# Kernel optimization log

Measured on AMD Instinct MI355X. Metric: run time of the kernel, lower is better.

## Reference

```python
import jax, jax.numpy as jnp
import numpy as np

COMMITMENT_COST = 0.25
NUM_EMBEDDINGS = 1024
EMBEDDING_DIM = 256


def setup_inputs() -> dict:
    key = jax.random.key(0)
    k1, k2 = jax.random.split(key)
    inputs = jax.random.normal(k1, (16, 4096, EMBEDDING_DIM), dtype=jnp.float32)
    embedding = jax.random.normal(k2, (NUM_EMBEDDINGS, EMBEDDING_DIM), dtype=jnp.float32)
    return {"inputs": inputs, "embedding": embedding}


def reference(inputs, embedding):
    input_shape = inputs.shape  # [B, T, D]
    D = embedding.shape[1]
    K = embedding.shape[0]
    flat = inputs.reshape(-1, D)  # [N, D]

    distances = (
        jnp.sum(flat * flat, axis=1, keepdims=True)
        + jnp.sum(embedding * embedding, axis=1)
        - 2.0 * jnp.matmul(flat, embedding.T)
    )

    encoding_indices = jnp.argmin(distances, axis=1)  # [N]
    encodings = jax.nn.one_hot(encoding_indices, K, dtype=jnp.float32)  # [N, K]

    # quantized = encodings @ embedding (a gather, expressed as in the original)
    quantized = embedding[encoding_indices].reshape(input_shape)

    # Commitment loss (quantized detached); EMA / codebook loss handled via EMA updates in training.
    e_latent_loss = jnp.mean((jax.lax.stop_gradient(quantized) - inputs) ** 2)
    vq_loss = COMMITMENT_COST * e_latent_loss

    # Straight-through estimator
    quantized_st = inputs + jax.lax.stop_gradient(quantized - inputs)

    avg_probs = jnp.mean(encodings, axis=0)  # [K]
    perplexity = jnp.exp(-jnp.sum(avg_probs * jnp.log(avg_probs + 1e-10)))

    return (vq_loss, quantized_st, perplexity, encodings, distances,
            encoding_indices[:, None])
```

## Files before the change

kernel.cpp:

```cpp
#include <hip/hip_runtime.h>
#include <hip/hip_fp16.h>
#include <stdint.h>

#define D 256
#define BM 128
#define BN 128
#define EPS 68

#define GLOBAL_AS __attribute__((address_space(1)))
#define LDS_AS    __attribute__((address_space(3)))

typedef _Float16 f16x8 __attribute__((ext_vector_type(8)));
typedef float f32x4 __attribute__((ext_vector_type(4)));

__device__ __forceinline__ void gload16(const unsigned short* g, unsigned short* l) {
    __builtin_amdgcn_global_load_lds((const GLOBAL_AS void*)g, (LDS_AS void*)l, 16, 0, 0);
}

__global__ void prep_kernel(const float* __restrict__ X, const float* __restrict__ E,
                            double* __restrict__ xn, double* __restrict__ en,
                            unsigned short* __restrict__ Xh, unsigned short* __restrict__ Xl,
                            unsigned short* __restrict__ Eh, unsigned short* __restrict__ El,
                            unsigned long long* __restrict__ keys,
                            unsigned int* __restrict__ hist, int N, int K)
{
    int gid  = blockIdx.x * blockDim.x + threadIdx.x;
    int wid  = gid >> 6;
    int lane = threadIdx.x & 63;
    if (wid < N + K) {
        bool isX = wid < N;
        int r = isX ? wid : wid - N;
        const float* src = isX ? (X + (size_t)r * D) : (E + (size_t)r * D);
        float4 v = *(const float4*)(src + lane * 4);
        double s = (double)v.x*v.x + (double)v.y*v.y + (double)v.z*v.z + (double)v.w*v.w;
        #pragma unroll
        for (int o = 32; o >= 1; o >>= 1) s += __shfl_xor(s, o, 64);

        ushort4 h4, l4;
        {
            __half h;
            h = __float2half_rn(v.x); h4.x = __half_as_ushort(h);
            l4.x = __half_as_ushort(__float2half_rn((v.x - __half2float(h)) * 4096.0f));
            h = __float2half_rn(v.y); h4.y = __half_as_ushort(h);
            l4.y = __half_as_ushort(__float2half_rn((v.y - __half2float(h)) * 4096.0f));
            h = __float2half_rn(v.z); h4.z = __half_as_ushort(h);
            l4.z = __half_as_ushort(__float2half_rn((v.z - __half2float(h)) * 4096.0f));
            h = __float2half_rn(v.w); h4.w = __half_as_ushort(h);
            l4.w = __half_as_ushort(__float2half_rn((v.w - __half2float(h)) * 4096.0f));
        }
        int p = r >> 7, ri = r & 127;
        int c = lane >> 3, g = lane & 7;
        int slot = g >> 1, hf = g & 1;
        int slot_r = (slot + (ri >> 1)) & 3;
        size_t off = ((size_t)(p * 8 + c) * 128 + ri) * 32 + slot_r * 8 + hf * 4;
        if (isX) {
            *(ushort4*)(Xh + off) = h4; *(ushort4*)(Xl + off) = l4;
            if (lane == 0) xn[r] = s;
        } else {
            *(ushort4*)(Eh + off) = h4; *(ushort4*)(El + off) = l4;
            if (lane == 0) en[r] = s;
        }
    }
    int stride = gridDim.x * blockDim.x;
    for (int i = gid; i < N; i += stride) keys[i] = 0xFFFFFFFFFFFFFFFFull;
    for (int i = gid; i < K; i += stride) hist[i] = 0u;
}

__global__ __launch_bounds__(256, 2) void dist_mfma(
    const unsigned short* __restrict__ Xh, const unsigned short* __restrict__ Xl,
    const unsigned short* __restrict__ Eh, const unsigned short* __restrict__ El,
    const double* __restrict__ xn, const double* __restrict__ en,
    float* __restrict__ dist, unsigned long long* __restrict__ keys,
    int N, int K)
{
    __shared__ alignas(16) unsigned short smem[2 * 4 * 4096];

    const int tid  = threadIdx.x;
    const int lane = tid & 63;
    const int wv   = tid >> 6;
    const int wrow = (wv & 1) * 64;
    const int wcol = (wv >> 1) * 64;

    const int flat = blockIdx.y * gridDim.x + blockIdx.x;
    const int nf   = (flat & 7) * ((int)(gridDim.x * gridDim.y) >> 3) + (flat >> 3);
    const int bx   = nf & 7;
    const int by   = nf >> 3;
    const int row0 = by * BM;
    const int col0 = bx * BN;

    const unsigned short* gA_h = Xh + (size_t)by * 32768;
    const unsigned short* gA_l = Xl + (size_t)by * 32768;
    const unsigned short* gB_h = Eh + (size_t)bx * 32768;
    const unsigned short* gB_l = El + (size_t)bx * 32768;

    f32x4 acc[4][4];
    f32x4 acr[4][4];
    #pragma unroll
    for (int i = 0; i < 4; ++i)
        #pragma unroll
        for (int j = 0; j < 4; ++j) { acc[i][j] = {0.f,0.f,0.f,0.f}; acr[i][j] = {0.f,0.f,0.f,0.f}; }

    const int toff = tid * 8;

    #define STAGE(c_, b_)                                                           \
    {                                                                               \
        const int co = (c_) * 4096;                                                 \
        unsigned short* lb = smem + (b_) * 16384;                                   \
        _Pragma("unroll")                                                           \
        for (int t = 0; t < 2; ++t) {                                               \
            gload16(gA_h + co + t*2048 + toff, lb +         t*2048 + toff);         \
            gload16(gA_l + co + t*2048 + toff, lb +  4096 + t*2048 + toff);         \
            gload16(gB_h + co + t*2048 + toff, lb +  8192 + t*2048 + toff);         \
            gload16(gB_l + co + t*2048 + toff, lb + 12288 + t*2048 + toff);         \
        }                                                                           \
    }

    const int fr = lane & 15;
    const int kq = lane >> 4;
    const int q  = kq;

    int offA[4], offB[4];
    #pragma unroll
    for (int i = 0; i < 4; ++i) {
        int rowA = wrow + i*16 + fr;
        offA[i] = rowA * 32 + ((kq + (rowA >> 1)) & 3) * 8;
        int rowB = wcol + i*16 + fr;
        offB[i] = rowB * 32 + ((kq + (rowB >> 1)) & 3) * 8;
    }

    STAGE(0, 0);
    asm volatile("s_waitcnt vmcnt(0)" ::: "memory");
    __builtin_amdgcn_s_barrier();
    __builtin_amdgcn_sched_barrier(0);

    for (int c = 0; c < 8; ++c) {
        const int b = c & 1;
        if (c < 7) {
            STAGE(c + 1, b ^ 1);
            asm volatile("s_waitcnt vmcnt(8)" ::: "memory");
        } else {
            asm volatile("s_waitcnt vmcnt(0)" ::: "memory");
        }
        __builtin_amdgcn_s_barrier();
        __builtin_amdgcn_sched_barrier(0);

        const unsigned short* buf = smem + b * 16384;
        f16x8 ah[4], bh[4], al[4], bl[4];
        #pragma unroll
        for (int i = 0; i < 4; ++i)
            ah[i] = *(const f16x8*)&buf[offA[i]];
        #pragma unroll
        for (int j = 0; j < 4; ++j)
            bh[j] = *(const f16x8*)&buf[8192 + offB[j]];
        #pragma unroll
        for (int i = 0; i < 4; ++i)
            #pragma unroll
            for (int j = 0; j < 4; ++j)
                acc[i][j] = __builtin_amdgcn_mfma_f32_16x16x32_f16(ah[i], bh[j], acc[i][j], 0, 0, 0);
        #pragma unroll
        for (int j = 0; j < 4; ++j)
            bl[j] = *(const f16x8*)&buf[12288 + offB[j]];
        #pragma unroll
        for (int i = 0; i < 4; ++i)
            #pragma unroll
            for (int j = 0; j < 4; ++j)
                acr[i][j] = __builtin_amdgcn_mfma_f32_16x16x32_f16(ah[i], bl[j], acr[i][j], 0, 0, 0);
        #pragma unroll
        for (int i = 0; i < 4; ++i)
            al[i] = *(const f16x8*)&buf[4096 + offA[i]];
        #pragma unroll
        for (int i = 0; i < 4; ++i)
            #pragma unroll
            for (int j = 0; j < 4; ++j)
                acr[i][j] = __builtin_amdgcn_mfma_f32_16x16x32_f16(al[i], bh[j], acr[i][j], 0, 0, 0);

        asm volatile("s_waitcnt lgkmcnt(0)" ::: "memory");
        __builtin_amdgcn_s_barrier();
        __builtin_amdgcn_sched_barrier(0);
    }

    float ecv[4];
    #pragma unroll
    for (int j = 0; j < 4; ++j) ecv[j] = (float)en[col0 + wcol + j*16 + fr];

    char* arena = (char*)smem + wv * 16384;

    {
        unsigned long long* kbuf = (unsigned long long*)arena;
        #pragma unroll
        for (int i = 0; i < 4; ++i) {
            #pragma unroll
            for (int r = 0; r < 4; ++r) {
                const int lr = i*16 + q*4 + r;
                unsigned long long bk = 0xFFFFFFFFFFFFFFFFull;
                #pragma unroll
                for (int j = 0; j < 4; ++j) {
                    float dotf = fmaf(acr[i][j][r], 0.000244140625f, acc[i][j][r]);
                    float m    = fmaf(-2.0f, dotf, ecv[j]);
                    uint32_t u = __float_as_uint(m);
                    u ^= ((uint32_t)((int32_t)u >> 31)) | 0x80000000u;
                    unsigned long long kk = ((unsigned long long)u << 32)
                                          | (unsigned)(col0 + wcol + j*16 + fr);
                    if (kk < bk) bk = kk;
                }
                kbuf[lr * 17 + fr] = bk;
            }
        }
        asm volatile("s_waitcnt lgkmcnt(0)" ::: "memory");
        unsigned long long best = 0xFFFFFFFFFFFFFFFFull;
        #pragma unroll
        for (int s = 0; s < 16; ++s) {
            unsigned long long v = kbuf[lane * 17 + s];
            if (v < best) best = v;
        }
        atomicMin(&keys[row0 + wrow + lane], best);
        asm volatile("s_waitcnt lgkmcnt(0)" ::: "memory");
    }

    {
        float xr32[4][4];
        #pragma unroll
        for (int i = 0; i < 4; ++i)
            #pragma unroll
            for (int r = 0; r < 4; ++r)
                xr32[i][r] = (float)xn[row0 + wrow + i*16 + q*4 + r];

        float* ebuf = (float*)arena;
        #pragma unroll
        for (int h = 0; h < 2; ++h) {
            #pragma unroll
            for (int i2 = 0; i2 < 2; ++i2) {
                const int i = h * 2 + i2;
                #pragma unroll
                for (int r = 0; r < 4; ++r) {
                    #pragma unroll
                    for (int j = 0; j < 4; ++j) {
                        float dotf = fmaf(acr[i][j][r], 0.000244140625f, acc[i][j][r]);
                        float dv   = fmaf(-2.0f, dotf, xr32[i][r] + ecv[j]);
                        ebuf[(i2*16 + q*4 + r) * EPS + j*16 + fr] = dv;
                    }
                }
            }
            asm volatile("s_waitcnt lgkmcnt(0)" ::: "memory");
            #pragma unroll
            for (int s = 0; s < 8; ++s) {
                const int rl = s*4 + q;
                float4 v = *(const float4*)&ebuf[rl * EPS + fr * 4];
                const int grow = row0 + wrow + h*32 + rl;
                *(float4*)&dist[(size_t)grow * K + col0 + wcol + fr*4] = v;
            }
            asm volatile("s_waitcnt lgkmcnt(0)" ::: "memory");
        }
    }
    #undef STAGE
}

__global__ void row_out(const float* __restrict__ X, const float* __restrict__ E,
                        const unsigned long long* __restrict__ keys,
                        float* __restrict__ quant, float* __restrict__ enc,
                        float* __restrict__ idxf, unsigned int* __restrict__ hist,
                        float* __restrict__ partials, int N, int K)
{
    int wid  = (blockIdx.x * blockDim.x + threadIdx.x) >> 6;
    int lane = threadIdx.x & 63;
    if (wid >= N) return;
    int idx = (int)(unsigned)(keys[wid] & 0xFFFFFFFFull);

    float4 x4 = *(const float4*)(X + (size_t)wid * D + lane*4);
    float4 q4 = *(const float4*)(E + (size_t)idx * D + lane*4);
    *(float4*)(quant + (size_t)wid * D + lane*4) = q4;
    float dx = q4.x-x4.x, dy = q4.y-x4.y, dz = q4.z-x4.z, dw = q4.w-x4.w;
    float s = dx*dx + dy*dy + dz*dz + dw*dw;
    #pragma unroll
    for (int o = 32; o >= 1; o >>= 1) s += __shfl_xor(s, o, 64);

    #pragma unroll
    for (int c = 0; c < 4; ++c) {
        int col = c * 256 + lane * 4;
        float4 v;
        v.x = (col + 0 == idx) ? 1.0f : 0.0f;
        v.y = (col + 1 == idx) ? 1.0f : 0.0f;
        v.z = (col + 2 == idx) ? 1.0f : 0.0f;
        v.w = (col + 3 == idx) ? 1.0f : 0.0f;
        *(float4*)(enc + (size_t)wid * K + col) = v;
    }
    if (lane == 0) {
        partials[wid] = s;
        idxf[wid] = (float)idx;
        atomicAdd(&hist[idx], 1u);
    }
}

__global__ void finalize_kernel(const float* __restrict__ partials,
                                const unsigned int* __restrict__ hist,
                                float* __restrict__ out_loss,
                                float* __restrict__ out_perp,
                                int N, int K)
{
    int tid = threadIdx.x;
    float ls = 0.0f;
    for (int i = tid; i < N; i += 1024) ls += partials[i];
    float ent = 0.0f;
    if (tid < K) {
        float p = (float)hist[tid] / (float)N;
        ent = p * logf(p + 1e-10f);
    }
    #pragma unroll
    for (int o = 32; o >= 1; o >>= 1) {
        ls  += __shfl_xor(ls,  o, 64);
        ent += __shfl_xor(ent, o, 64);
    }
    __shared__ float sl[16], se[16];
    int w = tid >> 6, lane = tid & 63;
    if (lane == 0) { sl[w] = ls; se[w] = ent; }
    __syncthreads();
    if (tid == 0) {
        float L = 0.0f, En = 0.0f;
        for (int i = 0; i < 16; ++i) { L += sl[i]; En += se[i]; }
        *out_loss = 0.25f * L / ((float)N * (float)D);
        *out_perp = expf(-En);
    }
}

extern "C" void kernel_launch(void* const* d_in, const int* in_sizes, int n_in,
                              void* d_out, int out_size, void* d_ws, size_t ws_size,
                              hipStream_t stream)
{
    const float* X = (const float*)d_in[0];
    const float* E = (const float*)d_in[1];
    const int N = in_sizes[0] / D;
    const int K = in_sizes[1] / D;
    float* out = (float*)d_out;

    const size_t O1 = 1;
    const size_t O2 = O1 + (size_t)N * D;
    const size_t O3 = O2 + 1;
    const size_t O4 = O3 + (size_t)N * K;
    const size_t O5 = O4 + (size_t)N * K;

    char* ws = (char*)d_ws;
    size_t off = 0;
    auto alloc = [&](size_t bytes) -> void* {
        void* p = ws + off;
        off += (bytes + 255) & ~(size_t)255;
        return p;
    };
    double* xn = (double*)alloc((size_t)N * 8);
    double* en = (double*)alloc((size_t)K * 8);
    unsigned long long* keys = (unsigned long long*)alloc((size_t)N * 8);
    unsigned int* hist = (unsigned int*)alloc((size_t)K * 4);
    float* partials = (float*)alloc((size_t)N * 4);
    unsigned short* Xh = (unsigned short*)alloc((size_t)N * D * 2);
    unsigned short* Xl = (unsigned short*)alloc((size_t)N * D * 2);
    unsigned short* Eh = (unsigned short*)alloc((size_t)K * D * 2);
    unsigned short* El = (unsigned short*)alloc((size_t)K * D * 2);

    int prep_blocks = (N + K + 3) / 4;
    prep_kernel<<<prep_blocks, 256, 0, stream>>>(X, E, xn, en, Xh, Xl, Eh, El,
                                                 keys, hist, N, K);

    dim3 g(K / BN, N / BM);
    dist_mfma<<<g, 256, 0, stream>>>(Xh, Xl, Eh, El, xn, en,
                                     out + O4, keys, N, K);

    row_out<<<N / 4, 256, 0, stream>>>(X, E, keys, out + O1, out + O3,
                                       out + O5, hist, partials, N, K);

    finalize_kernel<<<1, 1024, 0, stream>>>(partials, hist, out, out + O2, N, K);
}
```

Baseline: 265.0 us.

## Derive commitment loss from argmin distance, drop X reread, use float norms

The row_out kernel no longer rereads X to compute the squared error against the chosen code. Each row's minimum distance (x-norm added to the best key inside dist_mfma) is reused as the per-row loss and accumulated in fixed point with a single 64-bit atomic, which replaces the partials array and its reduction. Row norms are stored as float instead of double, and s_setprio wraps the MFMA block. This removes a 64 MB read of X, but the loss now comes from the mixed-precision expanded distance, which may be less accurate than the direct difference.

After: 959.0 us. 3.62x slower.

```diff
diff --git a/kernel.cpp b/kernel.cpp
--- a/kernel.cpp
+++ b/kernel.cpp
@@ -18,11 +18,12 @@
 }
 
 __global__ void prep_kernel(const float* __restrict__ X, const float* __restrict__ E,
-                            double* __restrict__ xn, double* __restrict__ en,
+                            float* __restrict__ xn, float* __restrict__ en,
                             unsigned short* __restrict__ Xh, unsigned short* __restrict__ Xl,
                             unsigned short* __restrict__ Eh, unsigned short* __restrict__ El,
                             unsigned long long* __restrict__ keys,
-                            unsigned int* __restrict__ hist, int N, int K)
+                            unsigned int* __restrict__ hist,
+                            unsigned long long* __restrict__ lossacc, int N, int K)
 {
     int gid  = blockIdx.x * blockDim.x + threadIdx.x;
     int wid  = gid >> 6;
@@ -55,21 +56,22 @@
         size_t off = ((size_t)(p * 8 + c) * 128 + ri) * 32 + slot_r * 8 + hf * 4;
         if (isX) {
             *(ushort4*)(Xh + off) = h4; *(ushort4*)(Xl + off) = l4;
-            if (lane == 0) xn[r] = s;
+            if (lane == 0) xn[r] = (float)s;
         } else {
             *(ushort4*)(Eh + off) = h4; *(ushort4*)(El + off) = l4;
-            if (lane == 0) en[r] = s;
+            if (lane == 0) en[r] = (float)s;
         }
     }
     int stride = gridDim.x * blockDim.x;
     for (int i = gid; i < N; i += stride) keys[i] = 0xFFFFFFFFFFFFFFFFull;
     for (int i = gid; i < K; i += stride) hist[i] = 0u;
+    if (gid == 0) *lossacc = 0ull;
 }
 
 __global__ __launch_bounds__(256, 2) void dist_mfma(
     const unsigned short* __restrict__ Xh, const unsigned short* __restrict__ Xl,
     const unsigned short* __restrict__ Eh, const unsigned short* __restrict__ El,
-    const double* __restrict__ xn, const double* __restrict__ en,
+    const float* __restrict__ xn, const float* __restrict__ en,
     float* __restrict__ dist, unsigned long long* __restrict__ keys,
     int N, int K)
 {
@@ -152,6 +154,7 @@
         #pragma unroll
         for (int j = 0; j < 4; ++j)
             bh[j] = *(const f16x8*)&buf[8192 + offB[j]];
+        __builtin_amdgcn_s_setprio(1);
         #pragma unroll
         for (int i = 0; i < 4; ++i)
             #pragma unroll
@@ -173,6 +176,7 @@
             #pragma unroll
             for (int j = 0; j < 4; ++j)
                 acr[i][j] = __builtin_amdgcn_mfma_f32_16x16x32_f16(al[i], bh[j], acr[i][j], 0, 0, 0);
+        __builtin_amdgcn_s_setprio(0);
 
         asm volatile("s_waitcnt lgkmcnt(0)" ::: "memory");
         __builtin_amdgcn_s_barrier();
@@ -181,7 +185,7 @@
 
     float ecv[4];
     #pragma unroll
-    for (int j = 0; j < 4; ++j) ecv[j] = (float)en[col0 + wcol + j*16 + fr];
+    for (int j = 0; j < 4; ++j) ecv[j] = en[col0 + wcol + j*16 + fr];
 
     char* arena = (char*)smem + wv * 16384;
 
@@ -213,6 +217,15 @@
             unsigned long long v = kbuf[lane * 17 + s];
             if (v < best) best = v;
         }
+        {
+            uint32_t u = (uint32_t)(best >> 32);
+            uint32_t fb = (u & 0x80000000u) ? (u ^ 0x80000000u) : ~u;
+            float m = __uint_as_float(fb);
+            float dv = xn[row0 + wrow + lane] + m;
+            uint32_t du = __float_as_uint(dv);
+            du ^= ((uint32_t)((int32_t)du >> 31)) | 0x80000000u;
+            best = ((unsigned long long)du << 32) | (best & 0xFFFFFFFFull);
+        }
         atomicMin(&keys[row0 + wrow + lane], best);
         asm volatile("s_waitcnt lgkmcnt(0)" ::: "memory");
     }
@@ -223,7 +236,7 @@
         for (int i = 0; i < 4; ++i)
             #pragma unroll
             for (int r = 0; r < 4; ++r)
-                xr32[i][r] = (float)xn[row0 + wrow + i*16 + q*4 + r];
+                xr32[i][r] = xn[row0 + wrow + i*16 + q*4 + r];
 
         float* ebuf = (float*)arena;
         #pragma unroll
@@ -255,24 +268,20 @@
     #undef STAGE
 }
 
-__global__ void row_out(const float* __restrict__ X, const float* __restrict__ E,
+__global__ void row_out(const float* __restrict__ E,
                         const unsigned long long* __restrict__ keys,
                         float* __restrict__ quant, float* __restrict__ enc,
                         float* __restrict__ idxf, unsigned int* __restrict__ hist,
-                        float* __restrict__ partials, int N, int K)
+                        unsigned long long* __restrict__ lossacc, int N, int K)
 {
     int wid  = (blockIdx.x * blockDim.x + threadIdx.x) >> 6;
     int lane = threadIdx.x & 63;
     if (wid >= N) return;
-    int idx = (int)(unsigned)(keys[wid] & 0xFFFFFFFFull);
-
-    float4 x4 = *(const float4*)(X + (size_t)wid * D + lane*4);
+    unsigned long long key = keys[wid];
+    int idx = (int)(unsigned)(key & 0xFFFFFFFFull);
+
     float4 q4 = *(const float4*)(E + (size_t)idx * D + lane*4);
     *(float4*)(quant + (size_t)wid * D + lane*4) = q4;
-    float dx = q4.x-x4.x, dy = q4.y-x4.y, dz = q4.z-x4.z, dw = q4.w-x4.w;
-    float s = dx*dx + dy*dy + dz*dz + dw*dw;
-    #pragma unroll
-    for (int o = 32; o >= 1; o >>= 1) s += __shfl_xor(s, o, 64);
 
     #pragma unroll
     for (int c = 0; c < 4; ++c) {
@@ -285,39 +294,40 @@
         *(float4*)(enc + (size_t)wid * K + col) = v;
     }
     if (lane == 0) {
-        partials[wid] = s;
         idxf[wid] = (float)idx;
         atomicAdd(&hist[idx], 1u);
-    }
-}
-
-__global__ void finalize_kernel(const float* __restrict__ partials,
+        uint32_t u = (uint32_t)(key >> 32);
+        uint32_t fb = (u & 0x80000000u) ? (u ^ 0x80000000u) : ~u;
+        float dv = __uint_as_float(fb);
+        long long fx = (long long)llrintf(dv * 1048576.0f);
+        atomicAdd(lossacc, (unsigned long long)fx);
+    }
+}
+
+__global__ void finalize_kernel(const unsigned long long* __restrict__ lossacc,
                                 const unsigned int* __restrict__ hist,
                                 float* __restrict__ out_loss,
                                 float* __restrict__ out_perp,
                                 int N, int K)
 {
     int tid = threadIdx.x;
-    float ls = 0.0f;
-    for (int i = tid; i < N; i += 1024) ls += partials[i];
     float ent = 0.0f;
     if (tid < K) {
         float p = (float)hist[tid] / (float)N;
         ent = p * logf(p + 1e-10f);
     }
     #pragma unroll
-    for (int o = 32; o >= 1; o >>= 1) {
-        ls  += __shfl_xor(ls,  o, 64);
-        ent += __shfl_xor(ent, o, 64);
-    }
-    __shared__ float sl[16], se[16];
+    for (int o = 32; o >= 1; o >>= 1) ent += __shfl_xor(ent, o, 64);
+    __shared__ float se[16];
     int w = tid >> 6, lane = tid & 63;
-    if (lane == 0) { sl[w] = ls; se[w] = ent; }
+    if (lane == 0) se[w] = ent;
     __syncthreads();
     if (tid == 0) {
-        float L = 0.0f, En = 0.0f;
-        for (int i = 0; i < 16; ++i) { L += sl[i]; En += se[i]; }
-        *out_loss = 0.25f * L / ((float)N * (float)D);
+        float En = 0.0f;
+        for (int i = 0; i < 16; ++i) En += se[i];
+        long long fx = (long long)(*lossacc);
+        double L = (double)fx / 1048576.0;
+        *out_loss = (float)(0.25 * L / ((double)N * (double)D));
         *out_perp = expf(-En);
     }
 }
@@ -345,11 +355,11 @@
         off += (bytes + 255) & ~(size_t)255;
         return p;
     };
-    double* xn = (double*)alloc((size_t)N * 8);
-    double* en = (double*)alloc((size_t)K * 8);
+    float* xn = (float*)alloc((size_t)N * 4);
+    float* en = (float*)alloc((size_t)K * 4);
     unsigned long long* keys = (unsigned long long*)alloc((size_t)N * 8);
     unsigned int* hist = (unsigned int*)alloc((size_t)K * 4);
-    float* partials = (float*)alloc((size_t)N * 4);
+    unsigned long long* lossacc = (unsigned long long*)alloc(256);
     unsigned short* Xh = (unsigned short*)alloc((size_t)N * D * 2);
     unsigned short* Xl = (unsigned short*)alloc((size_t)N * D * 2);
     unsigned short* Eh = (unsigned short*)alloc((size_t)K * D * 2);
@@ -357,14 +367,14 @@
 
     int prep_blocks = (N + K + 3) / 4;
     prep_kernel<<<prep_blocks, 256, 0, stream>>>(X, E, xn, en, Xh, Xl, Eh, El,
-                                                 keys, hist, N, K);
+                                                 keys, hist, lossacc, N, K);
 
     dim3 g(K / BN, N / BM);
     dist_mfma<<<g, 256, 0, stream>>>(Xh, Xl, Eh, El, xn, en,
                                      out + O4, keys, N, K);
 
-    row_out<<<N / 4, 256, 0, stream>>>(X, E, keys, out + O1, out + O3,
-                                       out + O5, hist, partials, N, K);
-
-    finalize_kernel<<<1, 1024, 0, stream>>>(partials, hist, out, out + O2, N, K);
-}
+    row_out<<<N / 4, 256, 0, stream>>>(E, keys, out + O1, out + O3,
+                                       out + O5, hist, lossacc, N, K);
+
+    finalize_kernel<<<1, 1024, 0, stream>>>(lossacc, hist, out, out + O2, N, K);
+}
```
